# Kernel optimization log

Hardware: AMD Instinct MI355X
Metric: run time of the kernel (lower is better)

The kernel has to match this reference:

```python
import jax, jax.numpy as jnp
import numpy as np

N_NODES = 50000
N_EDGES = 800000
IN_CH = 64
OUT_CH = 32
HEADS = 4
NUM_EDGE_TYPES = 64


def _sincos_pe(max_len, d_model):
    pos = np.arange(max_len, dtype=np.float32)[:, None]
    div = np.exp(np.arange(0, d_model, 2, dtype=np.float32) * (-np.log(10000.0) / d_model))
    pe = np.zeros((max_len, d_model), dtype=np.float32)
    pe[:, 0::2] = np.sin(pos * div)
    pe[:, 1::2] = np.cos(pos * div)
    return jnp.asarray(pe)


def setup_inputs() -> dict:
    key = jax.random.key(0)
    k1, k2, k3, k4, k5, k6 = jax.random.split(key, 6)
    x = jax.random.uniform(k1, (N_NODES, IN_CH), dtype=jnp.float32)
    edge_index = jax.random.randint(k2, (2, N_EDGES), 0, N_NODES, dtype=jnp.int64)
    edge_type = jax.random.randint(k3, (N_EDGES,), 0, NUM_EDGE_TYPES, dtype=jnp.int64)
    pe = _sincos_pe(NUM_EDGE_TYPES, IN_CH)
    W = jax.random.normal(k4, (IN_CH, HEADS * OUT_CH), dtype=jnp.float32) * 0.1
    att_src = jax.random.normal(k5, (HEADS, OUT_CH), dtype=jnp.float32) * 0.1
    att_dst = jax.random.normal(k6, (HEADS, OUT_CH), dtype=jnp.float32) * 0.1
    bias = jnp.zeros((HEADS * OUT_CH,), dtype=jnp.float32)
    return {"x": x, "edge_index": edge_index, "edge_type": edge_type, "pe": pe,
            "W": W, "att_src": att_src, "att_dst": att_dst, "bias": bias}


def reference(x, edge_index, edge_type, pe, W, att_src, att_dst, bias):
    N = x.shape[0]
    H, C = att_src.shape
    src, dst = edge_index[0], edge_index[1]

    # edge-wise positional encoding scatter-added into source nodes
    x_pos = x.at[src].add(pe[edge_type])

    # GATConv (PyG defaults: add_self_loops=True, negative_slope=0.2, concat=True)
    xl = (x_pos @ W).reshape(N, H, C)              # [N, H, C]
    a_src = (xl * att_src[None]).sum(-1)           # [N, H]
    a_dst = (xl * att_dst[None]).sum(-1)           # [N, H]

    self_idx = jnp.arange(N)
    src2 = jnp.concatenate([src, self_idx])        # [E'] with self loops
    dst2 = jnp.concatenate([dst, self_idx])

    alpha = jax.nn.leaky_relu(a_src[src2] + a_dst[dst2], 0.2)   # [E', H]
    amax = jax.ops.segment_max(alpha, dst2, num_segments=N)     # per-target max
    ex = jnp.exp(alpha - amax[dst2])
    denom = jax.ops.segment_sum(ex, dst2, num_segments=N)
    coef = ex / denom[dst2]                                     # segment softmax

    out = jax.ops.segment_sum(coef[:, :, None] * xl[src2], dst2, num_segments=N)
    out = out.reshape(N, H * C) + bias
    return jax.nn.elu(out)
```

## Files before the change

kernel.cpp:

```cpp
#include <hip/hip_runtime.h>
#include <cstdint>
#include <cstddef>

#define N_NODES 50000
#define N_EDGES 800000
#define IN_CH   64
#define OC      128
#define HEADS   4
#define CH      32

#define NB      391
#define BCAP    2560
#define EPB     2048
#define HIST_BLOCKS ((N_EDGES + EPB - 1) / EPB)

#define SENTINEL N_NODES
#define LST_LEN  (N_EDGES + 4 * N_NODES)

typedef __attribute__((ext_vector_type(8))) short short8;
typedef __attribute__((ext_vector_type(4))) float f32x4;

static inline int ceil_div(int a, int b){ return (a + b - 1) / b; }

__device__ __forceinline__ float lrelu(float x){ return fmaxf(x, 0.2f * x); }

__device__ __forceinline__ float bf_lo(unsigned u){ return __uint_as_float(u << 16); }
__device__ __forceinline__ float bf_hi(unsigned u){ return __uint_as_float(u & 0xFFFF0000u); }

__device__ __forceinline__ unsigned pack_bf16(float x, float y){
  unsigned ux = __float_as_uint(x), uy = __float_as_uint(y);
  ux += 0x7FFFu + ((ux >> 16) & 1u);
  uy += 0x7FFFu + ((uy >> 16) & 1u);
  return (ux >> 16) | (uy & 0xFFFF0000u);
}

__global__ __launch_bounds__(256) void k_histA(const int* __restrict__ ei,
                                               const int* __restrict__ et,
                                               int* __restrict__ btail,
                                               unsigned* __restrict__ bbuf){
  __shared__ int cnt[784];
  __shared__ int lofs[784];
  __shared__ int gpos[784];
  __shared__ unsigned stage[2 * EPB];
  __shared__ int sred[256];
  int tid = threadIdx.x;
  for (int i = tid; i < 784; i += 256) cnt[i] = 0;
  __syncthreads();

  int e0 = blockIdx.x * EPB;
  unsigned ent[16];
  int rnk[16];
  short bck[16];
  #pragma unroll
  for (int j = 0; j < 8; ++j){
    int e = e0 + j * 256 + tid;
    bck[2 * j] = -1; bck[2 * j + 1] = -1;
    if (e < N_EDGES){
      int s = ei[e], d = ei[N_EDGES + e], t = et[e];
      int bd = d >> 7, bs = s >> 7;
      ent[2 * j]     = ((unsigned)bd << 23) | ((unsigned)(d & 127) << 16) | (unsigned)s;
      ent[2 * j + 1] = ((unsigned)bs << 23) | ((unsigned)(s & 127) << 16) | (unsigned)t;
      bck[2 * j]     = (short)bd;
      bck[2 * j + 1] = (short)(391 + bs);
      rnk[2 * j]     = atomicAdd(&cnt[bd], 1);
      rnk[2 * j + 1] = atomicAdd(&cnt[391 + bs], 1);
    }
  }
  __syncthreads();

  int v[4], pre[4], run = 0;
  #pragma unroll
  for (int i = 0; i < 4; ++i){
    int idx = tid * 4 + i;
    v[i] = (idx < 784) ? cnt[idx] : 0;
    pre[i] = run; run += v[i];
  }
  sred[tid] = run; __syncthreads();
  for (int off = 1; off < 256; off <<= 1){
    int t = (tid >= off) ? sred[tid - off] : 0;
    __syncthreads();
    sred[tid] += t;
    __syncthreads();
  }
  int toff = sred[tid] - run;
  #pragma unroll
  for (int i = 0; i < 4; ++i){
    int idx = tid * 4 + i;
    if (idx < 784) lofs[idx] = toff + pre[i];
  }
  __syncthreads();

  #pragma unroll
  for (int j = 0; j < 16; ++j){
    if (bck[j] >= 0) stage[lofs[bck[j]] + rnk[j]] = ent[j];
  }
  for (int b = tid; b < 782; b += 256){
    int c = cnt[b];
    gpos[b] = c ? atomicAdd(&btail[b], c) : 0;
  }
  __syncthreads();

  int totalD = lofs[391];
  int totalA = lofs[782];
  for (int i = tid; i < totalA; i += 256){
    unsigned e = stage[i];
    int b9 = (int)(e >> 23);
    int bc = (i < totalD) ? b9 : 391 + b9;
    int gp = gpos[bc] + (i - lofs[bc]);
    if (gp < BCAP) bbuf[(size_t)bc * BCAP + gp] = e;
  }
}

__global__ __launch_bounds__(256) void k_passB(const unsigned* __restrict__ bbuf,
                                               const int* __restrict__ btail,
                                               int* __restrict__ row_dst,
                                               unsigned short* __restrict__ lst,
                                               const float* __restrict__ x,
                                               const unsigned* __restrict__ Bh,
                                               const float* __restrict__ att_s,
                                               const float* __restrict__ att_d,
                                               float* __restrict__ a_src,
                                               float* __restrict__ a_dst,
                                               unsigned* __restrict__ xh){
  int g = blockIdx.x, tid = threadIdx.x;
  if (g < NB){
    __shared__ int cnt[128], sc[128], cur[128], red[256];
    __shared__ int sbase;
    int d0 = g << 7;
    int nn = min(128, N_NODES - d0);
    int cnt_b = min(btail[g], BCAP);
    int part = 0;
    for (int q = tid; q < g; q += 256) part += min(btail[q], BCAP);
    red[tid] = part; __syncthreads();
    for (int off = 128; off > 0; off >>= 1){
      if (tid < off) red[tid] += red[tid + off];
      __syncthreads();
    }
    if (tid == 0) sbase = red[0];
    if (tid < 128) cnt[tid] = 0;
    __syncthreads();
    int base0 = sbase + 4 * d0;
    for (int i = tid; i < cnt_b; i += 256)
      atomicAdd(&cnt[(bbuf[(size_t)g * BCAP + i] >> 16) & 127], 1);
    __syncthreads();
    if (tid < 128) sc[tid] = cnt[tid];
    __syncthreads();
    for (int off = 1; off < 128; off <<= 1){
      int t = (tid < 128 && tid >= off) ? sc[tid - off] : 0;
      __syncthreads();
      if (tid < 128) sc[tid] += t;
      __syncthreads();
    }
    if (tid < nn){
      int ex = sc[tid] - cnt[tid];
      cur[tid] = ex + 4 * tid;
      row_dst[d0 + tid] = base0 + ex + 4 * tid;
    }
    if (g == NB - 1 && tid == 0) row_dst[N_NODES] = base0 + cnt_b + 4 * nn;
    __syncthreads();
    for (int i = tid; i < cnt_b; i += 256){
      unsigned e = bbuf[(size_t)g * BCAP + i];
      int p = atomicAdd(&cur[(e >> 16) & 127], 1);
      lst[base0 + p] = (unsigned short)(e & 0xFFFFu);
    }
    __syncthreads();
    if (tid < nn){
      int pe_ = cur[tid];
      #pragma unroll
      for (int k = 0; k < 4; ++k) lst[base0 + pe_ + k] = (unsigned short)SENTINEL;
    }
  } else {
    __shared__ unsigned hist[128 * 16];
    __shared__ unsigned sB[8192];
    __shared__ unsigned sA[4096];
    int n0 = (g - NB) << 7;
    for (int i = tid; i < 2048; i += 256) hist[i] = 0;
    __syncthreads();
    int cnt_b = min(btail[g], BCAP);
    for (int i = tid; i < cnt_b; i += 256){
      unsigned e = bbuf[(size_t)g * BCAP + i];
      unsigned t = e & 63u;
      atomicAdd(&hist[((e >> 16) & 127) * 16 + (t >> 2)], 1u << (8 * (t & 3)));
    }
    {
      const uint4* srcp = (const uint4*)Bh;
      uint4* dstp = (uint4*)sB;
      #pragma unroll
      for (int i = 0; i < 8; ++i) dstp[tid + i * 256] = srcp[tid + i * 256];
    }
    __syncthreads();

    int wid = tid >> 6, l = tid & 63;
    int c15 = l & 15, kq = l >> 4;
    float asv[8], adv[8];
    #pragma unroll
    for (int nt = 0; nt < 8; ++nt){
      asv[nt] = att_s[nt * 16 + c15];
      adv[nt] = att_d[nt * 16 + c15];
    }

    for (int half = 0; half < 2; ++half){
      int row0 = n0 + half * 64;
      {
        int r = tid >> 2, q = tid & 3;
        int n = row0 + r;
        unsigned swz = (unsigned)((r & 7) << 4);
        float4 xv[4];
        if (n < N_NODES){
          const float4* xr = (const float4*)(x + (size_t)n * 64);
          #pragma unroll
          for (int i = 0; i < 4; ++i) xv[i] = xr[q * 4 + i];
        } else {
          #pragma unroll
          for (int i = 0; i < 4; ++i) xv[i] = make_float4(0.f, 0.f, 0.f, 0.f);
        }
        unsigned pk[8];
        #pragma unroll
        for (int i = 0; i < 4; ++i){
          pk[2 * i]     = pack_bf16(xv[i].x, xv[i].y);
          pk[2 * i + 1] = pack_bf16(xv[i].z, xv[i].w);
        }
        unsigned b0 = (unsigned)(r * 256 + q * 32);
        *(uint4*)(sA + (((b0)      ^ swz) >> 2)) = make_uint4(pk[0], pk[1], pk[2], pk[3]);
        *(uint4*)(sA + (((b0 + 16) ^ swz) >> 2)) = make_uint4(pk[4], pk[5], pk[6], pk[7]);
        unsigned cw[4];
        #pragma unroll
        for (int i = 0; i < 4; ++i) cw[i] = hist[(half * 64 + r) * 16 + q * 4 + i];
        unsigned pc[8];
        #pragma unroll
        for (int i = 0; i < 4; ++i){
          unsigned w = cw[i];
          pc[2 * i]     = pack_bf16((float)(w & 0xFFu), (float)((w >> 8) & 0xFFu));
          pc[2 * i + 1] = pack_bf16((float)((w >> 16) & 0xFFu), (float)(w >> 24));
        }
        unsigned b1 = (unsigned)(r * 256 + 128 + q * 32);
        *(uint4*)(sA + (((b1)      ^ swz) >> 2)) = make_uint4(pc[0], pc[1], pc[2], pc[3]);
        *(uint4*)(sA + (((b1 + 16) ^ swz) >> 2)) = make_uint4(pc[4], pc[5], pc[6], pc[7]);
      }
      __syncthreads();

      int arow = wid * 16 + c15;
      f32x4 acc[8];
      #pragma unroll
      for (int nt = 0; nt < 8; ++nt) acc[nt] = (f32x4){0.f, 0.f, 0.f, 0.f};
      #pragma unroll
      for (int kk = 0; kk < 4; ++kk){
        unsigned abyte = (unsigned)(arow * 256 + kk * 64 + kq * 16);
        abyte ^= (unsigned)((arow & 7) << 4);
        short8 af = *(const short8*)((const char*)sA + abyte);
        #pragma unroll
        for (int nt = 0; nt < 8; ++nt){
          short8 bf = *(const short8*)(sB + (size_t)((nt * 4 + kk) * 64 + l) * 4);
          acc[nt] = __builtin_amdgcn_mfma_f32_16x16x32_bf16(af, bf, acc[nt], 0, 0, 0);
        }
      }

      #pragma unroll
      for (int r = 0; r < 4; ++r){
        int row = row0 + wid * 16 + kq * 4 + r;
        bool valid = row < N_NODES;
        #pragma unroll
        for (int h = 0; h < 4; ++h){
          float ps = acc[2 * h][r] * asv[2 * h] + acc[2 * h + 1][r] * asv[2 * h + 1];
          float pd = acc[2 * h][r] * adv[2 * h] + acc[2 * h + 1][r] * adv[2 * h + 1];
          #pragma unroll
          for (int m = 1; m < 16; m <<= 1){
            ps += __shfl_xor(ps, m);
            pd += __shfl_xor(pd, m);
          }
          if (valid && c15 == 0){
            a_src[row * 4 + h] = ps;
            a_dst[row * 4 + h] = pd;
          }
        }
        #pragma unroll
        for (int nt = 0; nt < 8; ++nt){
          float own = acc[nt][r];
          float nb = __shfl_xor(own, 1);
          if (valid && !(c15 & 1))
            xh[(size_t)row * 64 + nt * 8 + (c15 >> 1)] = pack_bf16(own, nb);
        }
      }
      __syncthreads();
    }
  }
}

__global__ __launch_bounds__(256) void k_prep(const float* __restrict__ pe,
                                              const float* __restrict__ W,
                                              unsigned* __restrict__ Bh,
                                              int* __restrict__ btail,
                                              float* __restrict__ a_src,
                                              unsigned* __restrict__ xh,
                                              unsigned short* __restrict__ lst){
  __shared__ float sPe[64 * 64];
  __shared__ float sW64[64 * 16];
  __shared__ float sPeW[64 * 16];
  int tid = threadIdx.x;
  int nt = blockIdx.x;
  int n0 = nt * 16;
  if (nt == 0){
    for (int i = tid; i < 1024; i += 256) btail[i] = 0;
    if (tid < 64) xh[(size_t)SENTINEL * 64 + tid] = 0;
    if (tid < 4)  a_src[SENTINEL * 4 + tid] = -1e30f;
    if (tid < 32) lst[LST_LEN + tid] = (unsigned short)SENTINEL;
  }
  for (int i = tid; i < 1024; i += 256)
    ((float4*)sPe)[i] = ((const float4*)pe)[i];
  for (int i = tid; i < 1024; i += 256){
    int k = i >> 4, j = i & 15;
    sW64[i] = W[k * 128 + n0 + j];
  }
  __syncthreads();
  for (int i = tid; i < 1024; i += 256){
    int t = i >> 4, j = i & 15;
    float a = 0.f;
    #pragma unroll
    for (int k = 0; k < 64; ++k) a += sPe[t * 64 + k] * sW64[k * 16 + j];
    sPeW[i] = a;
  }
  __syncthreads();
  for (int m = tid; m < 1024; m += 256){
    int j2 = m & 3, l = (m >> 2) & 63, kk = m >> 8;
    int k = kk * 32 + (l >> 4) * 8 + 2 * j2;
    int jl = l & 15;
    float v0, v1;
    if (k < 64){ v0 = sW64[k * 16 + jl]; v1 = sW64[(k + 1) * 16 + jl]; }
    else       { v0 = sPeW[(k - 64) * 16 + jl]; v1 = sPeW[(k - 63) * 16 + jl]; }
    Bh[nt * 1024 + m] = pack_bf16(v0, v1);
  }
}

__global__ __launch_bounds__(256) void k_aggregate(const int* __restrict__ row_dst,
                                                   const unsigned short* __restrict__ lst,
                                                   const float* __restrict__ a_src,
                                                   const float* __restrict__ a_dst,
                                                   const unsigned* __restrict__ xh,
                                                   const float* __restrict__ bias,
                                                   float* __restrict__ out){
  int n = (blockIdx.x * blockDim.x + threadIdx.x) >> 6;
  if (n >= N_NODES) return;
  int l = threadIdx.x & 63;
  int h = l >> 4;
  float ad = a_dst[n * 4 + h];

  float w = __expf(lrelu(a_src[n * 4 + h] + ad));
  unsigned uv = xh[(size_t)n * 64 + l];
  float l0 = w, l1 = 0.f, l2 = 0.f, l3 = 0.f;
  float a0x = w * bf_lo(uv), a0y = w * bf_hi(uv);
  float a1x = 0.f, a1y = 0.f, a2x = 0.f, a2y = 0.f, a3x = 0.f, a3y = 0.f;

  int k0 = row_dst[n];
  int k1 = row_dst[n + 1] - 4;

  int sA = (int)lst[k0], sB = (int)lst[k0 + 1], sC = (int)lst[k0 + 2], sD = (int)lst[k0 + 3];
  unsigned uA = xh[(size_t)sA * 64 + l]; float bA = a_src[sA * 4 + h];
  unsigned uB = xh[(size_t)sB * 64 + l]; float bB = a_src[sB * 4 + h];
  unsigned uC = xh[(size_t)sC * 64 + l]; float bC = a_src[sC * 4 + h];
  unsigned uD = xh[(size_t)sD * 64 + l]; float bD = a_src[sD * 4 + h];

  for (int j = k0; j < k1; j += 4){
    int nsA = (int)lst[j + 4], nsB = (int)lst[j + 5];
    int nsC = (int)lst[j + 6], nsD = (int)lst[j + 7];
    unsigned nuA = xh[(size_t)nsA * 64 + l]; float nbA = a_src[nsA * 4 + h];
    unsigned nuB = xh[(size_t)nsB * 64 + l]; float nbB = a_src[nsB * 4 + h];
    unsigned nuC = xh[(size_t)nsC * 64 + l]; float nbC = a_src[nsC * 4 + h];
    unsigned nuD = xh[(size_t)nsD * 64 + l]; float nbD = a_src[nsD * 4 + h];
    float wA = __expf(lrelu(bA + ad));
    l0 += wA;
    a0x = fmaf(wA, bf_lo(uA), a0x); a0y = fmaf(wA, bf_hi(uA), a0y);
    float wB = __expf(lrelu(bB + ad));
    l1 += wB;
    a1x = fmaf(wB, bf_lo(uB), a1x); a1y = fmaf(wB, bf_hi(uB), a1y);
    float wC = __expf(lrelu(bC + ad));
    l2 += wC;
    a2x = fmaf(wC, bf_lo(uC), a2x); a2y = fmaf(wC, bf_hi(uC), a2y);
    float wD = __expf(lrelu(bD + ad));
    l3 += wD;
    a3x = fmaf(wD, bf_lo(uD), a3x); a3y = fmaf(wD, bf_hi(uD), a3y);
    uA = nuA; bA = nbA; uB = nuB; bB = nbB;
    uC = nuC; bC = nbC; uD = nuD; bD = nbD;
  }
  float lsum = (l0 + l1) + (l2 + l3);
  float accx = (a0x + a1x) + (a2x + a3x);
  float accy = (a0y + a1y) + (a2y + a3y);
  float2 b = ((const float2*)bias)[l];
  float r0 = accx / lsum + b.x;
  float r1 = accy / lsum + b.y;
  float2 o;
  o.x = r0 > 0.f ? r0 : expm1f(r0);
  o.y = r1 > 0.f ? r1 : expm1f(r1);
  ((float2*)out)[(size_t)n * 64 + l] = o;
}

extern "C" void kernel_launch(void* const* d_in, const int* in_sizes, int n_in,
                              void* d_out, int out_size, void* d_ws, size_t ws_size,
                              hipStream_t stream){
  const float* x     = (const float*)d_in[0];
  const int*   ei    = (const int*)d_in[1];
  const int*   et    = (const int*)d_in[2];
  const float* pe    = (const float*)d_in[3];
  const float* W     = (const float*)d_in[4];
  const float* att_s = (const float*)d_in[5];
  const float* att_d = (const float*)d_in[6];
  const float* bias  = (const float*)d_in[7];
  float* out = (float*)d_out;

  int*      btail   = (int*)d_ws;
  int*      row_dst = btail + 1024;
  unsigned* Bh      = (unsigned*)(row_dst + N_NODES + 8);
  float*    a_src   = (float*)(Bh + 8192);
  float*    a_dst   = a_src + (size_t)(N_NODES + 1) * 4;
  unsigned* xh      = (unsigned*)(a_dst + (size_t)N_NODES * 4);
  unsigned* bbuf    = xh + (size_t)(N_NODES + 1) * 64;
  unsigned short* lst = (unsigned short*)(bbuf + (size_t)2 * NB * BCAP);

  const int B = 256;

  k_prep<<<8, B, 0, stream>>>(pe, W, Bh, btail, a_src, xh, lst);
  k_histA<<<HIST_BLOCKS, B, 0, stream>>>(ei, et, btail, bbuf);
  k_passB<<<2 * NB, B, 0, stream>>>(bbuf, btail, row_dst, lst,
                                    x, Bh, att_s, att_d, a_src, a_dst, xh);
  k_aggregate<<<ceil_div(N_NODES * 64, B), B, 0, stream>>>(row_dst, lst, a_src, a_dst,
                                                           xh, bias, out);
}
```

Baseline: 103.0 us.

## Merge prep into histogram kernel and deepen gather prefetch in aggregate

The small weight-prep kernel is folded into the histogram kernel as extra blocks, with the bucket-tail zeroing moved to a memset. This removes one dependent launch and lets the prep work overlap the histogram. The aggregate loop now prefetches two groups of four neighbours ahead instead of one, which keeps more gathers in flight at the cost of more registers. The new loop is guarded by k0 < k1, a case the old loop skipped anyway, and it reads lst up to index j+11, which relies on the sentinel padding.

```diff
diff --git a/kernel.cpp b/kernel.cpp
--- a/kernel.cpp
+++ b/kernel.cpp
@@ -34,80 +34,126 @@
   return (ux >> 16) | (uy & 0xFFFF0000u);
 }
 
-__global__ __launch_bounds__(256) void k_histA(const int* __restrict__ ei,
-                                               const int* __restrict__ et,
-                                               int* __restrict__ btail,
-                                               unsigned* __restrict__ bbuf){
-  __shared__ int cnt[784];
-  __shared__ int lofs[784];
-  __shared__ int gpos[784];
-  __shared__ unsigned stage[2 * EPB];
-  __shared__ int sred[256];
+__global__ __launch_bounds__(256) void k_hist_prep(const int* __restrict__ ei,
+                                                   const int* __restrict__ et,
+                                                   const float* __restrict__ pe,
+                                                   const float* __restrict__ W,
+                                                   unsigned* __restrict__ Bh,
+                                                   int* __restrict__ btail,
+                                                   unsigned* __restrict__ bbuf,
+                                                   float* __restrict__ a_src,
+                                                   unsigned* __restrict__ xh,
+                                                   unsigned short* __restrict__ lst){
+  __shared__ __align__(16) char smem[26816];
   int tid = threadIdx.x;
-  for (int i = tid; i < 784; i += 256) cnt[i] = 0;
-  __syncthreads();
-
-  int e0 = blockIdx.x * EPB;
-  unsigned ent[16];
-  int rnk[16];
-  short bck[16];
-  #pragma unroll
-  for (int j = 0; j < 8; ++j){
-    int e = e0 + j * 256 + tid;
-    bck[2 * j] = -1; bck[2 * j + 1] = -1;
-    if (e < N_EDGES){
-      int s = ei[e], d = ei[N_EDGES + e], t = et[e];
-      int bd = d >> 7, bs = s >> 7;
-      ent[2 * j]     = ((unsigned)bd << 23) | ((unsigned)(d & 127) << 16) | (unsigned)s;
-      ent[2 * j + 1] = ((unsigned)bs << 23) | ((unsigned)(s & 127) << 16) | (unsigned)t;
-      bck[2 * j]     = (short)bd;
-      bck[2 * j + 1] = (short)(391 + bs);
-      rnk[2 * j]     = atomicAdd(&cnt[bd], 1);
-      rnk[2 * j + 1] = atomicAdd(&cnt[391 + bs], 1);
-    }
-  }
-  __syncthreads();
-
-  int v[4], pre[4], run = 0;
-  #pragma unroll
-  for (int i = 0; i < 4; ++i){
-    int idx = tid * 4 + i;
-    v[i] = (idx < 784) ? cnt[idx] : 0;
-    pre[i] = run; run += v[i];
-  }
-  sred[tid] = run; __syncthreads();
-  for (int off = 1; off < 256; off <<= 1){
-    int t = (tid >= off) ? sred[tid - off] : 0;
-    __syncthreads();
-    sred[tid] += t;
-    __syncthreads();
-  }
-  int toff = sred[tid] - run;
-  #pragma unroll
-  for (int i = 0; i < 4; ++i){
-    int idx = tid * 4 + i;
-    if (idx < 784) lofs[idx] = toff + pre[i];
-  }
-  __syncthreads();
-
-  #pragma unroll
-  for (int j = 0; j < 16; ++j){
-    if (bck[j] >= 0) stage[lofs[bck[j]] + rnk[j]] = ent[j];
-  }
-  for (int b = tid; b < 782; b += 256){
-    int c = cnt[b];
-    gpos[b] = c ? atomicAdd(&btail[b], c) : 0;
-  }
-  __syncthreads();
-
-  int totalD = lofs[391];
-  int totalA = lofs[782];
-  for (int i = tid; i < totalA; i += 256){
-    unsigned e = stage[i];
-    int b9 = (int)(e >> 23);
-    int bc = (i < totalD) ? b9 : 391 + b9;
-    int gp = gpos[bc] + (i - lofs[bc]);
-    if (gp < BCAP) bbuf[(size_t)bc * BCAP + gp] = e;
+
+  if (blockIdx.x < HIST_BLOCKS){
+    int* cnt  = (int*)smem;
+    int* lofs = cnt + 784;
+    int* gpos = lofs + 784;
+    unsigned* stage = (unsigned*)(gpos + 784);
+    int* sred = (int*)(stage + 4096);
+
+    for (int i = tid; i < 784; i += 256) cnt[i] = 0;
+    __syncthreads();
+
+    int e0 = blockIdx.x * EPB;
+    unsigned ent[16];
+    int rnk[16];
+    short bck[16];
+    #pragma unroll
+    for (int j = 0; j < 8; ++j){
+      int e = e0 + j * 256 + tid;
+      bck[2 * j] = -1; bck[2 * j + 1] = -1;
+      if (e < N_EDGES){
+        int s = ei[e], d = ei[N_EDGES + e], t = et[e];
+        int bd = d >> 7, bs = s >> 7;
+        ent[2 * j]     = ((unsigned)bd << 23) | ((unsigned)(d & 127) << 16) | (unsigned)s;
+        ent[2 * j + 1] = ((unsigned)bs << 23) | ((unsigned)(s & 127) << 16) | (unsigned)t;
+        bck[2 * j]     = (short)bd;
+        bck[2 * j + 1] = (short)(391 + bs);
+        rnk[2 * j]     = atomicAdd(&cnt[bd], 1);
+        rnk[2 * j + 1] = atomicAdd(&cnt[391 + bs], 1);
+      }
+    }
+    __syncthreads();
+
+    int v[4], pre[4], run = 0;
+    #pragma unroll
+    for (int i = 0; i < 4; ++i){
+      int idx = tid * 4 + i;
+      v[i] = (idx < 784) ? cnt[idx] : 0;
+      pre[i] = run; run += v[i];
+    }
+    sred[tid] = run; __syncthreads();
+    for (int off = 1; off < 256; off <<= 1){
+      int t = (tid >= off) ? sred[tid - off] : 0;
+      __syncthreads();
+      sred[tid] += t;
+      __syncthreads();
+    }
+    int toff = sred[tid] - run;
+    #pragma unroll
+    for (int i = 0; i < 4; ++i){
+      int idx = tid * 4 + i;
+      if (idx < 784) lofs[idx] = toff + pre[i];
+    }
+    __syncthreads();
+
+    #pragma unroll
+    for (int j = 0; j < 16; ++j){
+      if (bck[j] >= 0) stage[lofs[bck[j]] + rnk[j]] = ent[j];
+    }
+    for (int b = tid; b < 782; b += 256){
+      int c = cnt[b];
+      gpos[b] = c ? atomicAdd(&btail[b], c) : 0;
+    }
+    __syncthreads();
+
+    int totalD = lofs[391];
+    int totalA = lofs[782];
+    for (int i = tid; i < totalA; i += 256){
+      unsigned e = stage[i];
+      int b9 = (int)(e >> 23);
+      int bc = (i < totalD) ? b9 : 391 + b9;
+      int gp = gpos[bc] + (i - lofs[bc]);
+      if (gp < BCAP) bbuf[(size_t)bc * BCAP + gp] = e;
+    }
+  } else {
+    float* sPe  = (float*)smem;
+    float* sW64 = sPe + 4096;
+    float* sPeW = sW64 + 1024;
+    int nt = blockIdx.x - HIST_BLOCKS;
+    int n0 = nt * 16;
+    if (nt == 0){
+      if (tid < 64) xh[(size_t)SENTINEL * 64 + tid] = 0;
+      if (tid < 4)  a_src[SENTINEL * 4 + tid] = -1e30f;
+      if (tid < 32) lst[LST_LEN + tid] = (unsigned short)SENTINEL;
+    }
+    for (int i = tid; i < 1024; i += 256)
+      ((float4*)sPe)[i] = ((const float4*)pe)[i];
+    for (int i = tid; i < 1024; i += 256){
+      int k = i >> 4, j = i & 15;
+      sW64[i] = W[k * 128 + n0 + j];
+    }
+    __syncthreads();
+    for (int i = tid; i < 1024; i += 256){
+      int t = i >> 4, j = i & 15;
+      float a = 0.f;
+      #pragma unroll
+      for (int k = 0; k < 64; ++k) a += sPe[t * 64 + k] * sW64[k * 16 + j];
+      sPeW[i] = a;
+    }
+    __syncthreads();
+    for (int m = tid; m < 1024; m += 256){
+      int j2 = m & 3, l = (m >> 2) & 63, kk = m >> 8;
+      int k = kk * 32 + (l >> 4) * 8 + 2 * j2;
+      int jl = l & 15;
+      float v0, v1;
+      if (k < 64){ v0 = sW64[k * 16 + jl]; v1 = sW64[(k + 1) * 16 + jl]; }
+      else       { v0 = sPeW[(k - 64) * 16 + jl]; v1 = sPeW[(k - 63) * 16 + jl]; }
+      Bh[nt * 1024 + m] = pack_bf16(v0, v1);
+    }
   }
 }
 
@@ -286,51 +332,6 @@
   }
 }
 
-__global__ __launch_bounds__(256) void k_prep(const float* __restrict__ pe,
-                                              const float* __restrict__ W,
-                                              unsigned* __restrict__ Bh,
-                                              int* __restrict__ btail,
-                                              float* __restrict__ a_src,
-                                              unsigned* __restrict__ xh,
-                                              unsigned short* __restrict__ lst){
-  __shared__ float sPe[64 * 64];
-  __shared__ float sW64[64 * 16];
-  __shared__ float sPeW[64 * 16];
-  int tid = threadIdx.x;
-  int nt = blockIdx.x;
-  int n0 = nt * 16;
-  if (nt == 0){
-    for (int i = tid; i < 1024; i += 256) btail[i] = 0;
-    if (tid < 64) xh[(size_t)SENTINEL * 64 + tid] = 0;
-    if (tid < 4)  a_src[SENTINEL * 4 + tid] = -1e30f;
-    if (tid < 32) lst[LST_LEN + tid] = (unsigned short)SENTINEL;
-  }
-  for (int i = tid; i < 1024; i += 256)
-    ((float4*)sPe)[i] = ((const float4*)pe)[i];
-  for (int i = tid; i < 1024; i += 256){
-    int k = i >> 4, j = i & 15;
-    sW64[i] = W[k * 128 + n0 + j];
-  }
-  __syncthreads();
-  for (int i = tid; i < 1024; i += 256){
-    int t = i >> 4, j = i & 15;
-    float a = 0.f;
-    #pragma unroll
-    for (int k = 0; k < 64; ++k) a += sPe[t * 64 + k] * sW64[k * 16 + j];
-    sPeW[i] = a;
-  }
-  __syncthreads();
-  for (int m = tid; m < 1024; m += 256){
-    int j2 = m & 3, l = (m >> 2) & 63, kk = m >> 8;
-    int k = kk * 32 + (l >> 4) * 8 + 2 * j2;
-    int jl = l & 15;
-    float v0, v1;
-    if (k < 64){ v0 = sW64[k * 16 + jl]; v1 = sW64[(k + 1) * 16 + jl]; }
-    else       { v0 = sPeW[(k - 64) * 16 + jl]; v1 = sPeW[(k - 63) * 16 + jl]; }
-    Bh[nt * 1024 + m] = pack_bf16(v0, v1);
-  }
-}
-
 __global__ __launch_bounds__(256) void k_aggregate(const int* __restrict__ row_dst,
                                                    const unsigned short* __restrict__ lst,
                                                    const float* __restrict__ a_src,
@@ -353,34 +354,50 @@
   int k0 = row_dst[n];
   int k1 = row_dst[n + 1] - 4;
 
-  int sA = (int)lst[k0], sB = (int)lst[k0 + 1], sC = (int)lst[k0 + 2], sD = (int)lst[k0 + 3];
-  unsigned uA = xh[(size_t)sA * 64 + l]; float bA = a_src[sA * 4 + h];
-  unsigned uB = xh[(size_t)sB * 64 + l]; float bB = a_src[sB * 4 + h];
-  unsigned uC = xh[(size_t)sC * 64 + l]; float bC = a_src[sC * 4 + h];
-  unsigned uD = xh[(size_t)sD * 64 + l]; float bD = a_src[sD * 4 + h];
-
-  for (int j = k0; j < k1; j += 4){
-    int nsA = (int)lst[j + 4], nsB = (int)lst[j + 5];
-    int nsC = (int)lst[j + 6], nsD = (int)lst[j + 7];
-    unsigned nuA = xh[(size_t)nsA * 64 + l]; float nbA = a_src[nsA * 4 + h];
-    unsigned nuB = xh[(size_t)nsB * 64 + l]; float nbB = a_src[nsB * 4 + h];
-    unsigned nuC = xh[(size_t)nsC * 64 + l]; float nbC = a_src[nsC * 4 + h];
-    unsigned nuD = xh[(size_t)nsD * 64 + l]; float nbD = a_src[nsD * 4 + h];
-    float wA = __expf(lrelu(bA + ad));
-    l0 += wA;
-    a0x = fmaf(wA, bf_lo(uA), a0x); a0y = fmaf(wA, bf_hi(uA), a0y);
-    float wB = __expf(lrelu(bB + ad));
-    l1 += wB;
-    a1x = fmaf(wB, bf_lo(uB), a1x); a1y = fmaf(wB, bf_hi(uB), a1y);
-    float wC = __expf(lrelu(bC + ad));
-    l2 += wC;
-    a2x = fmaf(wC, bf_lo(uC), a2x); a2y = fmaf(wC, bf_hi(uC), a2y);
-    float wD = __expf(lrelu(bD + ad));
-    l3 += wD;
-    a3x = fmaf(wD, bf_lo(uD), a3x); a3y = fmaf(wD, bf_hi(uD), a3y);
-    uA = nuA; bA = nbA; uB = nuB; bB = nbB;
-    uC = nuC; bC = nbC; uD = nuD; bD = nbD;
+  #define LOADB(U0,B0,U1,B1,U2,B2,U3,B3, base) {                          \
+    int t0 = (int)lst[(base)],     t1 = (int)lst[(base) + 1];             \
+    int t2 = (int)lst[(base) + 2], t3 = (int)lst[(base) + 3];             \
+    U0 = xh[(size_t)t0 * 64 + l];  B0 = a_src[t0 * 4 + h];                \
+    U1 = xh[(size_t)t1 * 64 + l];  B1 = a_src[t1 * 4 + h];                \
+    U2 = xh[(size_t)t2 * 64 + l];  B2 = a_src[t2 * 4 + h];                \
+    U3 = xh[(size_t)t3 * 64 + l];  B3 = a_src[t3 * 4 + h];                \
   }
+  #define PROC4(U0,B0,U1,B1,U2,B2,U3,B3) {                                \
+    float w0 = __expf(lrelu(B0 + ad));                                    \
+    l0 += w0; a0x = fmaf(w0, bf_lo(U0), a0x); a0y = fmaf(w0, bf_hi(U0), a0y); \
+    float w1 = __expf(lrelu(B1 + ad));                                    \
+    l1 += w1; a1x = fmaf(w1, bf_lo(U1), a1x); a1y = fmaf(w1, bf_hi(U1), a1y); \
+    float w2 = __expf(lrelu(B2 + ad));                                    \
+    l2 += w2; a2x = fmaf(w2, bf_lo(U2), a2x); a2y = fmaf(w2, bf_hi(U2), a2y); \
+    float w3 = __expf(lrelu(B3 + ad));                                    \
+    l3 += w3; a3x = fmaf(w3, bf_lo(U3), a3x); a3y = fmaf(w3, bf_hi(U3), a3y); \
+  }
+
+  unsigned uA0, uA1, uA2, uA3, uB0, uB1, uB2, uB3, n0_, n1_, n2_, n3_;
+  float bA0, bA1, bA2, bA3, bB0, bB1, bB2, bB3, f0_, f1_, f2_, f3_;
+
+  if (k0 < k1){
+    int j = k0;
+    LOADB(uA0,bA0, uA1,bA1, uA2,bA2, uA3,bA3, j);
+    LOADB(uB0,bB0, uB1,bB1, uB2,bB2, uB3,bB3, j + 4);
+    for (;;){
+      LOADB(n0_,f0_, n1_,f1_, n2_,f2_, n3_,f3_, j + 8);
+      PROC4(uA0,bA0, uA1,bA1, uA2,bA2, uA3,bA3);
+      uA0 = n0_; bA0 = f0_; uA1 = n1_; bA1 = f1_;
+      uA2 = n2_; bA2 = f2_; uA3 = n3_; bA3 = f3_;
+      j += 4;
+      if (j >= k1) break;
+      LOADB(n0_,f0_, n1_,f1_, n2_,f2_, n3_,f3_, j + 8);
+      PROC4(uB0,bB0, uB1,bB1, uB2,bB2, uB3,bB3);
+      uB0 = n0_; bB0 = f0_; uB1 = n1_; bB1 = f1_;
+      uB2 = n2_; bB2 = f2_; uB3 = n3_; bB3 = f3_;
+      j += 4;
+      if (j >= k1) break;
+    }
+  }
+  #undef LOADB
+  #undef PROC4
+
   float lsum = (l0 + l1) + (l2 + l3);
   float accx = (a0x + a1x) + (a2x + a3x);
   float accy = (a0y + a1y) + (a2y + a3y);
@@ -417,8 +434,9 @@
 
   const int B = 256;
 
-  k_prep<<<8, B, 0, stream>>>(pe, W, Bh, btail, a_src, xh, lst);
-  k_histA<<<HIST_BLOCKS, B, 0, stream>>>(ei, et, btail, bbuf);
+  hipMemsetAsync(btail, 0, 1024 * sizeof(int), stream);
+  k_hist_prep<<<HIST_BLOCKS + 8, B, 0, stream>>>(ei, et, pe, W, Bh, btail, bbuf,
+                                                 a_src, xh, lst);
   k_passB<<<2 * NB, B, 0, stream>>>(bbuf, btail, row_dst, lst,
                                     x, Bh, att_s, att_d, a_src, a_dst, xh);
   k_aggregate<<<ceil_div(N_NODES * 64, B), B, 0, stream>>>(row_dst, lst, a_src, a_dst,
```

Result: no change. 101.2 us (-1.8%).
